# Kernel tuning notes

Hardware: AMD Instinct MI355X
Metric: run time of the kernel (lower is better)

Reference implementation:

```python
import jax, jax.numpy as jnp
import numpy as np

N = 10000      # nodes
E = 160000     # edges (before self-loops)
IN = 256
NEG_SLOPE = 0.2  # PyG GATConv default


def gat_layer(x, src, dst, W, a_src, a_dst, bias, heads, concat, n):
    # x: [n, in_dim]; W: [in_dim, heads*C]; a_src/a_dst: [heads, C]
    C = W.shape[1] // heads
    h = (x @ W).reshape(n, heads, C)                      # [n,H,C]
    es = jnp.einsum('nhc,hc->nh', h, a_src)               # [n,H]
    ed = jnp.einsum('nhc,hc->nh', h, a_dst)               # [n,H]
    e = jax.nn.leaky_relu(es[src] + ed[dst], NEG_SLOPE)   # [E,H]
    # segment softmax over destination node (every node has a self-loop)
    emax = jax.ops.segment_max(e, dst, num_segments=n)    # [n,H]
    al = jnp.exp(e - emax[dst])                           # [E,H]
    den = jax.ops.segment_sum(al, dst, num_segments=n)    # [n,H]
    al = al / den[dst]
    out = jax.ops.segment_sum(h[src] * al[:, :, None], dst, num_segments=n)  # [n,H,C]
    out = out.reshape(n, heads * C) if concat else out.mean(axis=1)
    return out + bias


def setup_inputs() -> dict:
    key = jax.random.key(0)
    ks = jax.random.split(key, 16)
    s = 0.05
    p = lambda k, shp: jax.random.normal(k, shp, dtype=jnp.float32) * s
    return {
        'x': jax.random.normal(ks[0], (N, IN), dtype=jnp.float32),
        'edge_index': jax.random.randint(ks[1], (2, E), 0, N, dtype=jnp.int64),
        'proj_w': p(ks[2], (IN, 512)), 'proj_b': jnp.zeros((512,), jnp.float32),
        'w1': p(ks[3], (512, 4 * 512)),  'as1': p(ks[4], (4, 512)), 'ad1': p(ks[5], (4, 512)),  'b1': jnp.zeros((2048,), jnp.float32),
        'w2': p(ks[6], (2048, 4 * 512)), 'as2': p(ks[7], (4, 512)), 'ad2': p(ks[8], (4, 512)),  'b2': jnp.zeros((2048,), jnp.float32),
        'w3': p(ks[9], (2048, 2 * 512)), 'as3': p(ks[10], (2, 512)), 'ad3': p(ks[11], (2, 512)), 'b3': jnp.zeros((512,), jnp.float32),
    }


def reference(x, edge_index, proj_w, proj_b, w1, as1, ad1, b1,
              w2, as2, ad2, b2, w3, as3, ad3, b3):
    n = x.shape[0]
    loops = jnp.arange(n, dtype=edge_index.dtype)
    src = jnp.concatenate([edge_index[0], loops])   # PyG add_self_loops=True
    dst = jnp.concatenate([edge_index[1], loops])
    h = x @ proj_w + proj_b                         # dropout is identity in eval
    h = gat_layer(h, src, dst, w1, as1, ad1, b1, 4, True, n)
    h = jax.nn.elu(h)
    h = gat_layer(h, src, dst, w2, as2, ad2, b2, 4, True, n)
    h = jax.nn.elu(h)
    h = gat_layer(h, src, dst, w3, as3, ad3, b3, 2, False, n)
    return h
```

## Files before the change

### kernel.cpp

```cpp
#include <hip/hip_runtime.h>
#include <hip/hip_bf16.h>
#include <math.h>

#define CDIV(a,b) (((a)+(b)-1)/(b))

typedef __bf16  bf16x8 __attribute__((ext_vector_type(8)));
typedef float   f32x4  __attribute__((ext_vector_type(4)));
typedef unsigned short u16x8 __attribute__((ext_vector_type(8)));
typedef unsigned short u16x4 __attribute__((ext_vector_type(4)));

__device__ __forceinline__ float bf2f(unsigned short u) {
    union { unsigned int i; float f; } x; x.i = ((unsigned int)u) << 16; return x.f;
}
__device__ __forceinline__ unsigned short f2bf(float f) {
    union { float f; unsigned int i; } x; x.f = f;
    unsigned int r = x.i + 0x7fff + ((x.i >> 16) & 1);
    return (unsigned short)(r >> 16);
}

__global__ void hist_kernel(const int* __restrict__ ei, int* __restrict__ deg,
                            int E, int Et) {
    int e = blockIdx.x * blockDim.x + threadIdx.x;
    if (e >= Et) return;
    int d = (e < E) ? ei[E + e] : (e - E);
    atomicAdd(&deg[d], 1);
}

__global__ void scan_kernel(const int* __restrict__ deg, int* __restrict__ off, int n) {
    __shared__ int wsum[16];
    __shared__ int carry_s;
    int t = threadIdx.x, lane = t & 63, wv = t >> 6;
    if (t == 0) carry_s = 0;
    __syncthreads();
    for (int base = 0; base < n; base += 1024) {
        int v = (base + t < n) ? deg[base + t] : 0;
        int x = v;
#pragma unroll
        for (int o = 1; o < 64; o <<= 1) {
            int y = __shfl_up(x, o);
            if (lane >= o) x += y;
        }
        if (lane == 63) wsum[wv] = x;
        __syncthreads();
        if (wv == 0 && lane < 16) {
            int s = wsum[lane];
#pragma unroll
            for (int o = 1; o < 16; o <<= 1) {
                int y = __shfl_up(s, o);
                if (lane >= o) s += y;
            }
            wsum[lane] = s;
        }
        __syncthreads();
        int wprev = (wv == 0) ? 0 : wsum[wv - 1];
        int incl = carry_s + wprev + x;
        if (base + t < n) off[base + t] = incl - v;
        __syncthreads();
        if (t == 1023) carry_s = incl;
        __syncthreads();
    }
    if (t == 0) off[n] = carry_s;
}

__global__ void scatter_kernel(const int* __restrict__ ei, const int* __restrict__ off,
                               int* __restrict__ cur, int* __restrict__ csr,
                               int E, int Et) {
    int e = blockIdx.x * blockDim.x + threadIdx.x;
    if (e >= Et) return;
    int s, d;
    if (e < E) { s = ei[e]; d = ei[E + e]; } else { s = e - E; d = s; }
    int pos = off[d] + atomicAdd(&cur[d], 1);
    csr[pos] = s;
}

__global__ void wt_transpose_kernel(const float* __restrict__ w,
                                    __hip_bfloat16* __restrict__ wt,
                                    int K, int N) {
    __shared__ float tile[32][33];
    int kb = blockIdx.x * 32, nb = blockIdx.y * 32;
    int tx = threadIdx.x & 31, ty = threadIdx.x >> 5;
    for (int i = ty; i < 32; i += 8)
        tile[i][tx] = w[(size_t)(kb + i) * N + nb + tx];
    __syncthreads();
    for (int i = ty; i < 32; i += 8)
        wt[(size_t)(nb + i) * K + kb + tx] = __float2bfloat16(tile[tx][i]);
}

__global__ void cvt_bf16_kernel(const float* __restrict__ in,
                                __hip_bfloat16* __restrict__ out, int total) {
    int i = blockIdx.x * blockDim.x + threadIdx.x;
    if (i < total) out[i] = __float2bfloat16(in[i]);
}

__global__ void beff_kernel(const float* __restrict__ pb, const float* __restrict__ w1,
                            float* __restrict__ beff, int N) {
    int j  = blockIdx.x * 256 + threadIdx.x;
    int k0 = blockIdx.y * 64;
    float s = 0.f;
#pragma unroll
    for (int k = 0; k < 64; k++)
        s = fmaf(pb[k0 + k], w1[(size_t)(k0 + k) * N + j], s);
    atomicAdd(&beff[j], s);
}

__device__ __forceinline__ void gload16(void* lds, const void* g) {
    __builtin_amdgcn_global_load_lds(
        (const __attribute__((address_space(1))) void*)g,
        (__attribute__((address_space(3))) void*)lds, 16, 0, 0);
}

__global__ __launch_bounds__(256) void gemm_bf16_kernel(
    const __hip_bfloat16* __restrict__ A,
    const __hip_bfloat16* __restrict__ BT,
    const float* __restrict__ bias,
    __hip_bfloat16* __restrict__ Cb,
    int M, int N, int K, int MB, int NB, int XT)
{
    __shared__ __align__(16) __hip_bfloat16 As[128 * 32];
    __shared__ __align__(16) __hip_bfloat16 Bs[128 * 32];

    const int bid  = blockIdx.x;
    const int xcd  = bid & 7;
    const int slot = bid >> 3;
    const int x_sub = slot / NB;
    const int yb    = slot - x_sub * NB;
    const int xb    = xcd * XT + x_sub;
    if (xb >= MB) return;

    const int tid = threadIdx.x;
    const int m0 = xb * 128, n0 = yb * 128;
    const int w = tid >> 6, l = tid & 63;
    const int wm = (w & 1) * 64, wn = (w >> 1) * 64;
    const int lm = l & 15, lq = l >> 4;

    f32x4 acc[4][4] = {};

    const int arow = tid >> 2;
    const int acol = (tid & 3) * 8;
    const __hip_bfloat16* Ag = A  + (size_t)(m0 + arow) * K + acol;
    const __hip_bfloat16* Bg = BT + (size_t)(n0 + arow) * K + acol;
    char* AsW = (char*)As + (w << 10);
    char* BsW = (char*)Bs + (w << 10);

    for (int k0 = 0; k0 < K; k0 += 32) {
        gload16(AsW,        Ag + k0);
        gload16(AsW + 4096, Ag + (size_t)64 * K + k0);
        gload16(BsW,        Bg + k0);
        gload16(BsW + 4096, Bg + (size_t)64 * K + k0);
        __syncthreads();
        bf16x8 af[4], bfr[4];
#pragma unroll
        for (int i = 0; i < 4; i++)
            af[i] = *(const bf16x8*)(As + (wm + i * 16 + lm) * 32 + lq * 8);
#pragma unroll
        for (int j = 0; j < 4; j++)
            bfr[j] = *(const bf16x8*)(Bs + (wn + j * 16 + lm) * 32 + lq * 8);
#pragma unroll
        for (int i = 0; i < 4; i++)
#pragma unroll
            for (int j = 0; j < 4; j++)
                acc[i][j] = __builtin_amdgcn_mfma_f32_16x16x32_bf16(
                    af[i], bfr[j], acc[i][j], 0, 0, 0);
        __syncthreads();
    }

#pragma unroll
    for (int i = 0; i < 4; i++) {
        int rb = m0 + wm + i * 16 + lq * 4;
#pragma unroll
        for (int r = 0; r < 4; r++) {
            int row = rb + r;
            if (row >= M) continue;
#pragma unroll
            for (int j = 0; j < 4; j++) {
                int col = n0 + wn + j * 16 + lm;
                float v = acc[i][j][r];
                if (bias) v += bias[col];
                Cb[(size_t)row * N + col] = __float2bfloat16(v);
            }
        }
    }
}

__global__ void esed_kernel(const __hip_bfloat16* __restrict__ h,
                            const float* __restrict__ a_src,
                            const float* __restrict__ a_dst,
                            float* __restrict__ es, float* __restrict__ ed, int H) {
    int nidx = blockIdx.x;
    int t = threadIdx.x;
    int head = t >> 6, lane = t & 63;
    const unsigned short* hp =
        (const unsigned short*)h + (size_t)nidx * H * 512 + head * 512 + lane * 8;
    const float* sp = a_src + head * 512 + lane * 8;
    const float* dp = a_dst + head * 512 + lane * 8;
    u16x8 hv = *(const u16x8*)hp;
    float4 s0 = *(const float4*)sp, s1 = *(const float4*)(sp + 4);
    float4 d0 = *(const float4*)dp, d1 = *(const float4*)(dp + 4);
    float hf[8];
#pragma unroll
    for (int k = 0; k < 8; k++) hf[k] = bf2f(hv[k]);
    float s = hf[0]*s0.x + hf[1]*s0.y + hf[2]*s0.z + hf[3]*s0.w
            + hf[4]*s1.x + hf[5]*s1.y + hf[6]*s1.z + hf[7]*s1.w;
    float d = hf[0]*d0.x + hf[1]*d0.y + hf[2]*d0.z + hf[3]*d0.w
            + hf[4]*d1.x + hf[5]*d1.y + hf[6]*d1.z + hf[7]*d1.w;
    for (int o = 32; o; o >>= 1) { s += __shfl_down(s, o); d += __shfl_down(d, o); }
    if (lane == 0) { es[nidx * H + head] = s; ed[nidx * H + head] = d; }
}

template<int H, int VEC, bool MEAN>
__global__ __launch_bounds__(256) void agg_kernel(
    const __hip_bfloat16* __restrict__ h, const float* __restrict__ es,
    const float* __restrict__ ed, const int* __restrict__ csr,
    const int* __restrict__ off, const float* __restrict__ bias,
    float* __restrict__ outF, __hip_bfloat16* __restrict__ outB, int do_elu)
{
    constexpr int HS = H * 512;
    __shared__ float red[MEAN ? 1024 : 1];
    int d = blockIdx.x, t = threadIdx.x;
    int c0 = t * VEC;
    int head = c0 >> 9;
    float edd = ed[d * H + head];
    int beg = off[d], end = off[d + 1];
    float acc[VEC];
#pragma unroll
    for (int k = 0; k < VEC; k++) acc[k] = 0.f;
    float den = 0.f;
    const unsigned short* hb = (const unsigned short*)h;

    int i = beg;
    for (; i + 3 < end; i += 4) {
        int   s[4];
        float wgt[4];
#pragma unroll
        for (int u = 0; u < 4; u++) {
            s[u] = csr[i + u];
            float e = es[s[u] * H + head] + edd;
            e = (e > 0.f) ? e : 0.2f * e;
            wgt[u] = __expf(e);
        }
        if constexpr (VEC == 8) {
            u16x8 v[4];
#pragma unroll
            for (int u = 0; u < 4; u++)
                v[u] = *(const u16x8*)(hb + (size_t)s[u] * HS + c0);
#pragma unroll
            for (int u = 0; u < 4; u++) {
                den += wgt[u];
#pragma unroll
                for (int k = 0; k < 8; k++) acc[k] = fmaf(wgt[u], bf2f(v[u][k]), acc[k]);
            }
        } else {
            u16x4 v[4];
#pragma unroll
            for (int u = 0; u < 4; u++)
                v[u] = *(const u16x4*)(hb + (size_t)s[u] * HS + c0);
#pragma unroll
            for (int u = 0; u < 4; u++) {
                den += wgt[u];
#pragma unroll
                for (int k = 0; k < VEC; k++) acc[k] = fmaf(wgt[u], bf2f(v[u][k]), acc[k]);
            }
        }
    }
    for (; i < end; i++) {
        int s0 = csr[i];
        float e0 = es[s0 * H + head] + edd;
        e0 = (e0 > 0.f) ? e0 : 0.2f * e0;
        float w0 = __expf(e0);
        den += w0;
        const unsigned short* hp0 = hb + (size_t)s0 * HS + c0;
        if constexpr (VEC == 8) {
            u16x8 v0 = *(const u16x8*)hp0;
#pragma unroll
            for (int k = 0; k < 8; k++) acc[k] = fmaf(w0, bf2f(v0[k]), acc[k]);
        } else {
            u16x4 v0 = *(const u16x4*)hp0;
#pragma unroll
            for (int k = 0; k < VEC; k++) acc[k] = fmaf(w0, bf2f(v0[k]), acc[k]);
        }
    }

    float inv = 1.f / den;
    if constexpr (!MEAN) {
        u16x8 ov;
#pragma unroll
        for (int k = 0; k < VEC; k++) {
            float v = acc[k] * inv + bias[c0 + k];
            if (do_elu) v = (v > 0.f) ? v : expm1f(v);
            ov[k] = f2bf(v);
        }
        *(u16x8*)((unsigned short*)outB + (size_t)d * HS + c0) = ov;
    } else {
#pragma unroll
        for (int k = 0; k < VEC; k++) red[c0 + k] = acc[k] * inv;
        __syncthreads();
        if (t < 128) {
#pragma unroll
            for (int k = 0; k < 4; k++) {
                int c = t * 4 + k;
                outF[(size_t)d * 512 + c] = 0.5f * (red[c] + red[c + 512]) + bias[c];
            }
        }
    }
}

extern "C" void kernel_launch(void* const* d_in, const int* in_sizes, int n_in,
                              void* d_out, int out_size, void* d_ws, size_t ws_size,
                              hipStream_t stream) {
    const float* x      = (const float*)d_in[0];
    const int*   ei     = (const int*)  d_in[1];
    const float* proj_w = (const float*)d_in[2];
    const float* proj_b = (const float*)d_in[3];
    const float* w1  = (const float*)d_in[4];
    const float* as1 = (const float*)d_in[5];
    const float* ad1 = (const float*)d_in[6];
    const float* b1  = (const float*)d_in[7];
    const float* w2  = (const float*)d_in[8];
    const float* as2 = (const float*)d_in[9];
    const float* ad2 = (const float*)d_in[10];
    const float* b2  = (const float*)d_in[11];
    const float* w3  = (const float*)d_in[12];
    const float* as3 = (const float*)d_in[13];
    const float* ad3 = (const float*)d_in[14];
    const float* b3  = (const float*)d_in[15];

    const int n    = in_sizes[0] / 256;
    const int E    = in_sizes[1] / 2;
    const int Et   = E + n;
    const int MB   = CDIV(n, 128);
    const int Mpad = MB * 128;
    const int XT   = CDIV(MB, 8);

    char* p = (char*)d_ws;
    auto carve = [&](size_t bytes) {
        void* r = (void*)p;
        p += (bytes + 255) & ~(size_t)255;
        return r;
    };
    __hip_bfloat16* h_bf    = (__hip_bfloat16*)carve((size_t)Mpad * 2048 * sizeof(__hip_bfloat16));
    __hip_bfloat16* act_bf  = (__hip_bfloat16*)carve((size_t)Mpad * 2048 * sizeof(__hip_bfloat16));
    __hip_bfloat16* x_bf    = (__hip_bfloat16*)carve((size_t)Mpad * 256 * sizeof(__hip_bfloat16));
    __hip_bfloat16* pw_bf   = (__hip_bfloat16*)carve((size_t)256 * 512 * sizeof(__hip_bfloat16));
    __hip_bfloat16* w1t     = (__hip_bfloat16*)carve((size_t)2048 * 512 * sizeof(__hip_bfloat16));
    __hip_bfloat16* w2t     = (__hip_bfloat16*)carve((size_t)2048 * 2048 * sizeof(__hip_bfloat16));
    __hip_bfloat16* w3t     = (__hip_bfloat16*)carve((size_t)1024 * 2048 * sizeof(__hip_bfloat16));
    __hip_bfloat16* w_efft  = (__hip_bfloat16*)carve((size_t)2048 * 256 * sizeof(__hip_bfloat16));
    float* b_eff = (float*)carve((size_t)2048 * sizeof(float));
    float* es  = (float*)carve((size_t)n * 4 * sizeof(float));
    float* ed  = (float*)carve((size_t)n * 4 * sizeof(float));
    int* deg = (int*)carve((size_t)n * sizeof(int));
    int* cur = (int*)carve((size_t)n * sizeof(int));
    int* off = (int*)carve((size_t)(n + 1) * sizeof(int));
    int* csr = (int*)carve((size_t)Et * sizeof(int));
    (void)ws_size; (void)n_in;

    hipMemsetAsync(deg, 0, n * sizeof(int), stream);
    hipMemsetAsync(cur, 0, n * sizeof(int), stream);
    hipMemsetAsync(b_eff, 0, 2048 * sizeof(float), stream);
    hist_kernel<<<CDIV(Et, 256), 256, 0, stream>>>(ei, deg, E, Et);
    scan_kernel<<<1, 1024, 0, stream>>>(deg, off, n);
    scatter_kernel<<<CDIV(Et, 256), 256, 0, stream>>>(ei, off, cur, csr, E, Et);

    wt_transpose_kernel<<<dim3(512 / 32, 2048 / 32), 256, 0, stream>>>(w1, w1t, 512, 2048);
    wt_transpose_kernel<<<dim3(2048 / 32, 2048 / 32),256, 0, stream>>>(w2, w2t, 2048, 2048);
    wt_transpose_kernel<<<dim3(2048 / 32, 1024 / 32),256, 0, stream>>>(w3, w3t, 2048, 1024);
    cvt_bf16_kernel<<<CDIV(256 * 512, 256), 256, 0, stream>>>(proj_w, pw_bf, 256 * 512);
    cvt_bf16_kernel<<<CDIV(n * 256, 256), 256, 0, stream>>>(x, x_bf, n * 256);

    gemm_bf16_kernel<<<8 * 2 * 2, 256, 0, stream>>>(
        w1t, pw_bf, nullptr, w_efft, 2048, 256, 512, 16, 2, 2);
    beff_kernel<<<dim3(2048 / 256, 512 / 64), 256, 0, stream>>>(proj_b, w1, b_eff, 2048);

    auto gemm_grid = [&](int NB) { return 8 * XT * NB; };

    gemm_bf16_kernel<<<gemm_grid(16), 256, 0, stream>>>(
        x_bf, w_efft, b_eff, h_bf, n, 2048, 256, MB, 16, XT);
    esed_kernel<<<n, 4 * 64, 0, stream>>>(h_bf, as1, ad1, es, ed, 4);
    agg_kernel<4, 8, false><<<n, 256, 0, stream>>>(h_bf, es, ed, csr, off, b1,
                                                   nullptr, act_bf, 1);

    gemm_bf16_kernel<<<gemm_grid(16), 256, 0, stream>>>(
        act_bf, w2t, nullptr, h_bf, n, 2048, 2048, MB, 16, XT);
    esed_kernel<<<n, 4 * 64, 0, stream>>>(h_bf, as2, ad2, es, ed, 4);
    agg_kernel<4, 8, false><<<n, 256, 0, stream>>>(h_bf, es, ed, csr, off, b2,
                                                   nullptr, act_bf, 1);

    gemm_bf16_kernel<<<gemm_grid(8), 256, 0, stream>>>(
        act_bf, w3t, nullptr, h_bf, n, 1024, 2048, MB, 8, XT);
    esed_kernel<<<n, 2 * 64, 0, stream>>>(h_bf, as3, ad3, es, ed, 2);
    agg_kernel<2, 4, true><<<n, 256, 0, stream>>>(h_bf, es, ed, csr, off, b3,
                                                  (float*)d_out, nullptr, 0);
}
```

Before: 674.4 us.

## Fuse attention-score dot products into GEMM epilogue and merge prep kernels

```diff
diff --git a/kernel.cpp b/kernel.cpp
--- a/kernel.cpp
+++ b/kernel.cpp
@@ -73,11 +73,19 @@
     csr[pos] = s;
 }
 
-__global__ void wt_transpose_kernel(const float* __restrict__ w,
-                                    __hip_bfloat16* __restrict__ wt,
-                                    int K, int N) {
+__global__ void prep_t_kernel(const float* __restrict__ wa, __hip_bfloat16* __restrict__ wta,
+                              const float* __restrict__ wb, __hip_bfloat16* __restrict__ wtb,
+                              const float* __restrict__ wc, __hip_bfloat16* __restrict__ wtc,
+                              int t0, int t1, int t2) {
     __shared__ float tile[32][33];
-    int kb = blockIdx.x * 32, nb = blockIdx.y * 32;
+    int bid = blockIdx.x;
+    const float* w; __hip_bfloat16* wt; int K, N, r;
+    if (bid < t0)      { w = wa; wt = wta; K = 512;  N = 2048; r = bid; }
+    else if (bid < t1) { w = wb; wt = wtb; K = 2048; N = 2048; r = bid - t0; }
+    else               { w = wc; wt = wtc; K = 2048; N = 1024; r = bid - t1; }
+    (void)t2;
+    int kt = K >> 5;
+    int kb = (r % kt) * 32, nb = (r / kt) * 32;
     int tx = threadIdx.x & 31, ty = threadIdx.x >> 5;
     for (int i = ty; i < 32; i += 8)
         tile[i][tx] = w[(size_t)(kb + i) * N + nb + tx];
@@ -86,10 +94,20 @@
         wt[(size_t)(nb + i) * K + kb + tx] = __float2bfloat16(tile[tx][i]);
 }
 
-__global__ void cvt_bf16_kernel(const float* __restrict__ in,
-                                __hip_bfloat16* __restrict__ out, int total) {
+__global__ void cvt2_kernel(const float* __restrict__ a, __hip_bfloat16* __restrict__ ao,
+                            int na4,
+                            const float* __restrict__ b, __hip_bfloat16* __restrict__ bo,
+                            int nb4) {
     int i = blockIdx.x * blockDim.x + threadIdx.x;
-    if (i < total) out[i] = __float2bfloat16(in[i]);
+    const float* src; __hip_bfloat16* dst; int idx;
+    if (i < na4) { src = a; dst = ao; idx = i * 4; }
+    else if (i < na4 + nb4) { src = b; dst = bo; idx = (i - na4) * 4; }
+    else return;
+    float4 v = *(const float4*)(src + idx);
+    dst[idx + 0] = __float2bfloat16(v.x);
+    dst[idx + 1] = __float2bfloat16(v.y);
+    dst[idx + 2] = __float2bfloat16(v.z);
+    dst[idx + 3] = __float2bfloat16(v.w);
 }
 
 __global__ void beff_kernel(const float* __restrict__ pb, const float* __restrict__ w1,
@@ -114,6 +132,8 @@
     const __hip_bfloat16* __restrict__ BT,
     const float* __restrict__ bias,
     __hip_bfloat16* __restrict__ Cb,
+    const float* __restrict__ a_src, const float* __restrict__ a_dst,
+    float* __restrict__ es, float* __restrict__ ed, int H,
     int M, int N, int K, int MB, int NB, int XT)
 {
     __shared__ __align__(16) __hip_bfloat16 As[128 * 32];
@@ -164,47 +184,49 @@
         __syncthreads();
     }
 
+    const int head = (n0 + wn) >> 9;
+    float as_[4], ad_[4];
+    if (a_src) {
+        int cb = ((n0 + wn) & 511) + lm;
+#pragma unroll
+        for (int j = 0; j < 4; j++) {
+            as_[j] = a_src[head * 512 + cb + j * 16];
+            ad_[j] = a_dst[head * 512 + cb + j * 16];
+        }
+    }
+
 #pragma unroll
     for (int i = 0; i < 4; i++) {
-        int rb = m0 + wm + i * 16 + lq * 4;
 #pragma unroll
         for (int r = 0; r < 4; r++) {
-            int row = rb + r;
-            if (row >= M) continue;
+            int row = m0 + wm + i * 16 + lq * 4 + r;
+            bool valid = row < M;
+            float v[4];
 #pragma unroll
             for (int j = 0; j < 4; j++) {
-                int col = n0 + wn + j * 16 + lm;
-                float v = acc[i][j][r];
-                if (bias) v += bias[col];
-                Cb[(size_t)row * N + col] = __float2bfloat16(v);
-            }
-        }
-    }
-}
-
-__global__ void esed_kernel(const __hip_bfloat16* __restrict__ h,
-                            const float* __restrict__ a_src,
-                            const float* __restrict__ a_dst,
-                            float* __restrict__ es, float* __restrict__ ed, int H) {
-    int nidx = blockIdx.x;
-    int t = threadIdx.x;
-    int head = t >> 6, lane = t & 63;
-    const unsigned short* hp =
-        (const unsigned short*)h + (size_t)nidx * H * 512 + head * 512 + lane * 8;
-    const float* sp = a_src + head * 512 + lane * 8;
-    const float* dp = a_dst + head * 512 + lane * 8;
-    u16x8 hv = *(const u16x8*)hp;
-    float4 s0 = *(const float4*)sp, s1 = *(const float4*)(sp + 4);
-    float4 d0 = *(const float4*)dp, d1 = *(const float4*)(dp + 4);
-    float hf[8];
-#pragma unroll
-    for (int k = 0; k < 8; k++) hf[k] = bf2f(hv[k]);
-    float s = hf[0]*s0.x + hf[1]*s0.y + hf[2]*s0.z + hf[3]*s0.w
-            + hf[4]*s1.x + hf[5]*s1.y + hf[6]*s1.z + hf[7]*s1.w;
-    float d = hf[0]*d0.x + hf[1]*d0.y + hf[2]*d0.z + hf[3]*d0.w
-            + hf[4]*d1.x + hf[5]*d1.y + hf[6]*d1.z + hf[7]*d1.w;
-    for (int o = 32; o; o >>= 1) { s += __shfl_down(s, o); d += __shfl_down(d, o); }
-    if (lane == 0) { es[nidx * H + head] = s; ed[nidx * H + head] = d; }
+                v[j] = acc[i][j][r];
+                if (bias) v[j] += bias[n0 + wn + j * 16 + lm];
+            }
+            if (valid) {
+#pragma unroll
+                for (int j = 0; j < 4; j++)
+                    Cb[(size_t)row * N + n0 + wn + j * 16 + lm] = __float2bfloat16(v[j]);
+            }
+            if (a_src) {
+                float se = v[0] * as_[0] + v[1] * as_[1] + v[2] * as_[2] + v[3] * as_[3];
+                float de = v[0] * ad_[0] + v[1] * ad_[1] + v[2] * ad_[2] + v[3] * ad_[3];
+#pragma unroll
+                for (int o = 1; o < 16; o <<= 1) {
+                    se += __shfl_xor(se, o);
+                    de += __shfl_xor(de, o);
+                }
+                if (lm == 0 && valid) {
+                    atomicAdd(&es[row * H + head], se);
+                    atomicAdd(&ed[row * H + head], de);
+                }
+            }
+        }
+    }
 }
 
 template<int H, int VEC, bool MEAN>
@@ -348,46 +370,47 @@
     float* b_eff = (float*)carve((size_t)2048 * sizeof(float));
     float* es  = (float*)carve((size_t)n * 4 * sizeof(float));
     float* ed  = (float*)carve((size_t)n * 4 * sizeof(float));
-    int* deg = (int*)carve((size_t)n * sizeof(int));
-    int* cur = (int*)carve((size_t)n * sizeof(int));
+    int* deg = (int*)carve((size_t)2 * n * sizeof(int));
+    int* cur = deg + n;
     int* off = (int*)carve((size_t)(n + 1) * sizeof(int));
     int* csr = (int*)carve((size_t)Et * sizeof(int));
     (void)ws_size; (void)n_in;
 
-    hipMemsetAsync(deg, 0, n * sizeof(int), stream);
-    hipMemsetAsync(cur, 0, n * sizeof(int), stream);
+    hipMemsetAsync(deg, 0, 2 * n * sizeof(int), stream);
     hipMemsetAsync(b_eff, 0, 2048 * sizeof(float), stream);
     hist_kernel<<<CDIV(Et, 256), 256, 0, stream>>>(ei, deg, E, Et);
     scan_kernel<<<1, 1024, 0, stream>>>(deg, off, n);
     scatter_kernel<<<CDIV(Et, 256), 256, 0, stream>>>(ei, off, cur, csr, E, Et);
 
-    wt_transpose_kernel<<<dim3(512 / 32, 2048 / 32), 256, 0, stream>>>(w1, w1t, 512, 2048);
-    wt_transpose_kernel<<<dim3(2048 / 32, 2048 / 32),256, 0, stream>>>(w2, w2t, 2048, 2048);
-    wt_transpose_kernel<<<dim3(2048 / 32, 1024 / 32),256, 0, stream>>>(w3, w3t, 2048, 1024);
-    cvt_bf16_kernel<<<CDIV(256 * 512, 256), 256, 0, stream>>>(proj_w, pw_bf, 256 * 512);
-    cvt_bf16_kernel<<<CDIV(n * 256, 256), 256, 0, stream>>>(x, x_bf, n * 256);
+    const int t0 = (512 / 32) * (2048 / 32);
+    const int t1 = t0 + (2048 / 32) * (2048 / 32);
+    const int t2 = t1 + (2048 / 32) * (1024 / 32);
+    prep_t_kernel<<<t2, 256, 0, stream>>>(w1, w1t, w2, w2t, w3, w3t, t0, t1, t2);
+    const int na4 = 256 * 512 / 4, nb4 = n * 256 / 4;
+    cvt2_kernel<<<CDIV(na4 + nb4, 256), 256, 0, stream>>>(proj_w, pw_bf, na4, x, x_bf, nb4);
 
     gemm_bf16_kernel<<<8 * 2 * 2, 256, 0, stream>>>(
-        w1t, pw_bf, nullptr, w_efft, 2048, 256, 512, 16, 2, 2);
+        w1t, pw_bf, nullptr, w_efft, nullptr, nullptr, nullptr, nullptr, 0,
+        2048, 256, 512, 16, 2, 2);
     beff_kernel<<<dim3(2048 / 256, 512 / 64), 256, 0, stream>>>(proj_b, w1, b_eff, 2048);
 
     auto gemm_grid = [&](int NB) { return 8 * XT * NB; };
 
+    hipMemsetAsync(es, 0, 2 * (size_t)n * 4 * sizeof(float), stream);
     gemm_bf16_kernel<<<gemm_grid(16), 256, 0, stream>>>(
-        x_bf, w_efft, b_eff, h_bf, n, 2048, 256, MB, 16, XT);
-    esed_kernel<<<n, 4 * 64, 0, stream>>>(h_bf, as1, ad1, es, ed, 4);
+        x_bf, w_efft, b_eff, h_bf, as1, ad1, es, ed, 4, n, 2048, 256, MB, 16, XT);
     agg_kernel<4, 8, false><<<n, 256, 0, stream>>>(h_bf, es, ed, csr, off, b1,
                                                    nullptr, act_bf, 1);
 
+    hipMemsetAsync(es, 0, 2 * (size_t)n * 4 * sizeof(float), stream);
     gemm_bf16_kernel<<<gemm_grid(16), 256, 0, stream>>>(
-        act_bf, w2t, nullptr, h_bf, n, 2048, 2048, MB, 16, XT);
-    esed_kernel<<<n, 4 * 64, 0, stream>>>(h_bf, as2, ad2, es, ed, 4);
+        act_bf, w2t, nullptr, h_bf, as2, ad2, es, ed, 4, n, 2048, 2048, MB, 16, XT);
     agg_kernel<4, 8, false><<<n, 256, 0, stream>>>(h_bf, es, ed, csr, off, b2,
                                                    nullptr, act_bf, 1);
 
+    hipMemsetAsync(es, 0, 2 * (size_t)n * 4 * sizeof(float), stream);
     gemm_bf16_kernel<<<gemm_grid(8), 256, 0, stream>>>(
-        act_bf, w3t, nullptr, h_bf, n, 1024, 2048, MB, 8, XT);
-    esed_kernel<<<n, 2 * 64, 0, stream>>>(h_bf, as3, ad3, es, ed, 2);
+        act_bf, w3t, nullptr, h_bf, as3, ad3, es, ed, 2, n, 1024, 2048, MB, 8, XT);
     agg_kernel<2, 4, true><<<n, 256, 0, stream>>>(h_bf, es, ed, csr, off, b3,
                                                   (float*)d_out, nullptr, 0);
 }
```

Result: slower. 743.8 us (+10.3%).
